# Optimization experiments

Hardware: AMD Instinct MI355X
Metric: run time of the kernel (lower is better)

Reference implementation:

```python
import jax, jax.numpy as jnp
import numpy as np

GRID_SIZE = 10
DEGREE = 3


def bspline_basis(x, grid_size=GRID_SIZE, degree=DEGREE):
    """Cox-de Boor B-spline basis on a uniform grid over [-1, 1].
    x: (...,) -> (..., grid_size + degree)
    """
    h = 2.0 / grid_size
    # extended knot vector, length grid_size + 2*degree + 1
    knots = jnp.arange(-degree, grid_size + degree + 1, dtype=x.dtype) * h - 1.0
    # keep inputs inside the grid support (standard KAN practice)
    x = jnp.clip(x, -1.0, 1.0 - 1e-6)
    xe = x[..., None]
    b = ((xe >= knots[:-1]) & (xe < knots[1:])).astype(x.dtype)  # degree-0, (..., K-1)
    for d in range(1, degree + 1):
        left = (xe - knots[: -(d + 1)]) / (knots[d:-1] - knots[: -(d + 1)]) * b[..., :-1]
        right = (knots[d + 1:] - xe) / (knots[d + 1:] - knots[1:-d]) * b[..., 1:]
        b = left + right
    return b  # (..., grid_size + degree)


def setup_inputs() -> dict:
    key = jax.random.key(0)
    k1, k2, k3 = jax.random.split(key, 3)
    B, S, IN, OUT, E = 4, 2048, 256, 256, 8
    n_basis = GRID_SIZE + DEGREE
    x = jax.random.normal(k1, (B, S, IN), dtype=jnp.float32)
    coeff = jax.random.normal(k2, (E, n_basis), dtype=jnp.float32) * 0.1
    gating_weights = jax.random.normal(k3, (IN, OUT, E), dtype=jnp.float32)
    return {"x": x, "coeff": coeff, "gating_weights": gating_weights}


def reference(x, coeff, gating_weights):
    # spline experts: elementwise basis eval, then per-expert linear combo
    basis = bspline_basis(x)                              # (B, S, I, n_basis)
    expert_outputs = jnp.einsum('bsin,en->bsie', basis, coeff)  # (B, S, I, E)
    gates = jax.nn.softmax(gating_weights, axis=-1)       # (I, O, E)
    out = jnp.einsum('bsie,ioe->bso', expert_outputs, gates)
    return out
```

## Files before the change

kernel.cpp:

```cpp
#include <hip/hip_runtime.h>

typedef __attribute__((ext_vector_type(8))) short short8;
typedef __attribute__((ext_vector_type(4))) float f32x4;

#define IN_DIM 256
#define OUT_DIM 256
#define NB 16
#define KDIM (IN_DIM * NB)
#define TM 128
#define TN 128
#define BK 64
#define KSPLIT 4
#define IPER (IN_DIM / KSPLIT)
#define STEPS (IPER / 4)

__device__ __forceinline__ unsigned short f2bf(float f) {
  union { float f; unsigned int u; } v; v.f = f;
  unsigned int r = v.u + 0x7fffu + ((v.u >> 16) & 1u);
  return (unsigned short)(r >> 16);
}

__device__ __forceinline__ void glds16(const void* g, void* l) {
  __builtin_amdgcn_global_load_lds((__attribute__((address_space(1))) const void*)g,
                                   (__attribute__((address_space(3))) void*)l, 16, 0, 0);
}

__device__ __forceinline__ void spline_row(float xv, unsigned* d) {
  float xc = fminf(fmaxf(xv, -1.0f), 1.0f - 1e-6f);
  float u = (xc + 1.0f) * 5.0f;
  int c = (int)u;
  c = c > 9 ? 9 : (c < 0 ? 0 : c);
  float tt = u - (float)c;
  float omt = 1.0f - tt;
  float t2 = tt * tt, t3 = t2 * tt;
  float b0 = omt * omt * omt * (1.0f / 6.0f);
  float b1 = (3.0f * t3 - 6.0f * t2 + 4.0f) * (1.0f / 6.0f);
  float b2 = (-3.0f * t3 + 3.0f * t2 + 3.0f * tt + 1.0f) * (1.0f / 6.0f);
  float b3 = t3 * (1.0f / 6.0f);
  unsigned h0 = f2bf(b0), h1 = f2bf(b1), h2 = f2bf(b2), h3 = f2bf(b3);
  const int a = c >> 1;
  const bool odd = (c & 1) != 0;
  unsigned p01 = h0 | (h1 << 16);
  unsigned p23 = h2 | (h3 << 16);
  unsigned A0 = odd ? (h0 << 16) : p01;
  unsigned A1 = odd ? (h1 | (h2 << 16)) : p23;
  unsigned A2 = odd ? h3 : 0u;
#pragma unroll
  for (int j = 0; j < 8; ++j) {
    unsigned v = (j == a) ? A0 : 0u;
    v = (j == a + 1) ? A1 : v;
    v = (j == a + 2) ? A2 : v;
    d[j] = v;
  }
}

__global__ __launch_bounds__(256) void kan_prep(const float* __restrict__ coeff,
                                                const float* __restrict__ gw,
                                                unsigned short* __restrict__ BmT,
                                                float* __restrict__ out) {
  __shared__ float csh[104];
  __shared__ unsigned short tile[16][256];
  const int t = threadIdx.x;
  {
    const int bid = blockIdx.y * 16 + blockIdx.x;
    float4 z; z.x = z.y = z.z = z.w = 0.f;
    float4* ob = (float4*)out;
#pragma unroll
    for (int j = 0; j < 8; ++j) ob[(size_t)bid * 2048 + j * 256 + t] = z;
  }
  if (t < 104) csh[t] = coeff[t];
  __syncthreads();
  const int otile = blockIdx.x, itile = blockIdx.y;
  const int il = t >> 4, ol = t & 15;
  const int i = itile * 16 + il;
  const int o = otile * 16 + ol;
  const float* g = gw + (size_t)(i * OUT_DIM + o) * 8;
  float4 g0 = *(const float4*)g;
  float4 g1 = *(const float4*)(g + 4);
  float ge[8] = {g0.x, g0.y, g0.z, g0.w, g1.x, g1.y, g1.z, g1.w};
  float mx = ge[0];
#pragma unroll
  for (int e = 1; e < 8; ++e) mx = fmaxf(mx, ge[e]);
  float p[8]; float s = 0.f;
#pragma unroll
  for (int e = 0; e < 8; ++e) { p[e] = __expf(ge[e] - mx); s += p[e]; }
  const float inv = 1.0f / s;
  unsigned short row[16];
#pragma unroll
  for (int n = 0; n < 13; ++n) {
    float w = 0.f;
#pragma unroll
    for (int e = 0; e < 8; ++e) w += p[e] * csh[e * 13 + n];
    row[n] = f2bf(w * inv);
  }
  row[13] = 0; row[14] = 0; row[15] = 0;
  int4* dst = (int4*)&tile[ol][il * 16];
  dst[0] = *(const int4*)&row[0];
  dst[1] = *(const int4*)&row[8];
  __syncthreads();
  const int oo = t >> 4, ck = t & 15;
  int4 v0 = *(const int4*)&tile[oo][ck * 16];
  int4 v1 = *(const int4*)&tile[oo][ck * 16 + 8];
  int4* out4 = (int4*)(BmT + (size_t)(otile * 16 + oo) * KDIM + itile * 256 + ck * 16);
  out4[0] = v0;
  out4[1] = v1;
}

#define STAGE_A(snext, buf) do {                                                   \
    const int p_ = (snext) & 1, h_ = ((snext) >> 1) & 1;                           \
    const char* xb_ = (const char*)&Xsh[0][0] + h_ * 4096;                         \
    float2 xv_ = *(const float2*)(xb_ + r * 32 + ((p_ ^ (r & 1)) << 4) + ph * 8);  \
    char* ab_ = (char*)&Ash[0][0] + (buf) * 16384 + r * 128;                       \
    const int m_ = r & 7;                                                          \
    unsigned d_[8];                                                                \
    spline_row(xv_.x, d_);                                                         \
    *(int4*)(ab_ + (((4 * ph + 0) ^ m_) << 4)) = *(const int4*)&d_[0];             \
    *(int4*)(ab_ + (((4 * ph + 1) ^ m_) << 4)) = *(const int4*)&d_[4];             \
    spline_row(xv_.y, d_);                                                         \
    *(int4*)(ab_ + (((4 * ph + 2) ^ m_) << 4)) = *(const int4*)&d_[0];             \
    *(int4*)(ab_ + (((4 * ph + 3) ^ m_) << 4)) = *(const int4*)&d_[4];             \
  } while (0)

__global__ __launch_bounds__(256, 2) void kan_gemm(const float* __restrict__ x,
                                                   const unsigned short* __restrict__ BmT,
                                                   float* __restrict__ out) {
  __shared__ unsigned short Ash[2][TM * BK];
  __shared__ unsigned short Bsh[2][TN * BK];
  __shared__ float Xsh[2][TM * 8];

  const int t = threadIdx.x;
  const int lane = t & 63;
  const int wave = t >> 6;
  const int wm = wave & 1, wn = wave >> 1;
  const int mb = blockIdx.x * TM;
  const int ob = blockIdx.y * TN;
  const int i0 = blockIdx.z * IPER;

  const int r = t & 127;
  const int ph = t >> 7;

  const int jsw = (t & 7) ^ ((t >> 3) & 7);
  const unsigned short* bgbase = BmT + (size_t)(ob + (t >> 3)) * KDIM + i0 * NB + jsw * 8;
  const int csw = (t & 1) ^ ((t >> 1) & 1);
  const float* xgbase = x + (size_t)(mb + (t >> 1)) * IN_DIM + i0 + csw * 4;

  char* const bl = (char*)&Bsh[0][0] + wave * 1024;
  char* const xl = (char*)&Xsh[0][0] + wave * 1024;

  f32x4 acc[4][4];
#pragma unroll
  for (int a = 0; a < 4; ++a)
#pragma unroll
    for (int b = 0; b < 4; ++b) acc[a][b] = (f32x4){0.f, 0.f, 0.f, 0.f};

  int aoff[4], boff[4];
#pragma unroll
  for (int f = 0; f < 4; ++f) {
    const int ro = wm * 64 + f * 16 + (lane & 15);
    aoff[f] = ro * 128 + ((((lane >> 4)) ^ (ro & 7)) << 4);
    const int bo = wn * 64 + f * 16 + (lane & 15);
    boff[f] = bo * 128 + ((((lane >> 4)) ^ (bo & 7)) << 4);
  }

  glds16(xgbase, xl);
#pragma unroll
  for (int q = 0; q < 4; ++q)
    glds16(bgbase + (size_t)q * 32 * KDIM, bl + q * 4096);
  asm volatile("s_waitcnt vmcnt(0)" ::: "memory");
  __syncthreads();
  STAGE_A(0, 0);

  for (int s = 0; s < STEPS; ++s) {
    __syncthreads();
    const int cur = s & 1;
    if (s + 1 < STEPS) {
#pragma unroll
      for (int q = 0; q < 4; ++q)
        glds16(bgbase + (size_t)(s + 1) * BK + (size_t)q * 32 * KDIM,
               bl + (1 - cur) * 16384 + q * 4096);
    }
    if (((s & 1) == 0) && (s + 2 < STEPS)) {
      const int g = (s >> 1) + 1;
      glds16(xgbase + g * 8, xl + (g & 1) * 4096);
    }
    const char* Ac = (const char*)&Ash[0][0] + cur * 16384;
    const char* Bc = (const char*)&Bsh[0][0] + cur * 16384;
    __builtin_amdgcn_s_setprio(1);
#pragma unroll
    for (int kc = 0; kc < 2; ++kc) {
      short8 af[4], bfr[4];
#pragma unroll
      for (int f = 0; f < 4; ++f) af[f] = *(const short8*)(Ac + (aoff[f] ^ (kc << 6)));
#pragma unroll
      for (int f = 0; f < 4; ++f) bfr[f] = *(const short8*)(Bc + (boff[f] ^ (kc << 6)));
#pragma unroll
      for (int mf = 0; mf < 4; ++mf)
#pragma unroll
        for (int nf = 0; nf < 4; ++nf)
          acc[mf][nf] = __builtin_amdgcn_mfma_f32_16x16x32_bf16(af[mf], bfr[nf], acc[mf][nf], 0, 0, 0);
    }
    __builtin_amdgcn_s_setprio(0);
    if (s + 1 < STEPS) STAGE_A(s + 1, 1 - cur);
  }

#pragma unroll
  for (int mf = 0; mf < 4; ++mf)
#pragma unroll
    for (int nf = 0; nf < 4; ++nf)
#pragma unroll
      for (int q = 0; q < 4; ++q) {
        int row = mb + wm * 64 + mf * 16 + ((lane >> 4) << 2) + q;
        int col = ob + wn * 64 + nf * 16 + (lane & 15);
        atomicAdd(out + (size_t)row * OUT_DIM + col, acc[mf][nf][q]);
      }
}

extern "C" void kernel_launch(void* const* d_in, const int* in_sizes, int n_in,
                              void* d_out, int out_size, void* d_ws, size_t ws_size,
                              hipStream_t stream) {
  const float* x     = (const float*)d_in[0];
  const float* coeff = (const float*)d_in[1];
  const float* gw    = (const float*)d_in[2];
  float* out = (float*)d_out;
  unsigned short* BmT = (unsigned short*)d_ws;

  kan_prep<<<dim3(16, 16), dim3(256), 0, stream>>>(coeff, gw, BmT, out);
  dim3 grid(8192 / TM, OUT_DIM / TN, KSPLIT);
  kan_gemm<<<grid, dim3(256), 0, stream>>>(x, BmT, out);
}
```

Before: 114.1 us.

## Drop split-K atomics; use small M tiles with full-K blocks and plain stores

Removes the K-split and atomic accumulation. Each block now handles a 32x128 output tile over the full input dimension and writes results with plain stores, so the output no longer needs zeroing in the prep kernel. The B operand is staged with a wider BK of 128. x is read directly from global memory per step instead of through LDS staging. The tiles are much smaller, which lowers MFMA reuse per block and increases redundant B-matrix loads across the larger number of blocks.

```diff
diff --git a/kernel.cpp b/kernel.cpp
--- a/kernel.cpp
+++ b/kernel.cpp
@@ -7,12 +7,12 @@
 #define OUT_DIM 256
 #define NB 16
 #define KDIM (IN_DIM * NB)
-#define TM 128
+#define TM 32
 #define TN 128
-#define BK 64
-#define KSPLIT 4
-#define IPER (IN_DIM / KSPLIT)
-#define STEPS (IPER / 4)
+#define BK 128
+#define STEPS (IN_DIM / 8)
+#define ABUF (TM * BK * 2)
+#define BBUF (TN * BK * 2)
 
 __device__ __forceinline__ unsigned short f2bf(float f) {
   union { float f; unsigned int u; } v; v.f = f;
@@ -56,18 +56,10 @@
 
 __global__ __launch_bounds__(256) void kan_prep(const float* __restrict__ coeff,
                                                 const float* __restrict__ gw,
-                                                unsigned short* __restrict__ BmT,
-                                                float* __restrict__ out) {
+                                                unsigned short* __restrict__ BmT) {
   __shared__ float csh[104];
   __shared__ unsigned short tile[16][256];
   const int t = threadIdx.x;
-  {
-    const int bid = blockIdx.y * 16 + blockIdx.x;
-    float4 z; z.x = z.y = z.z = z.w = 0.f;
-    float4* ob = (float4*)out;
-#pragma unroll
-    for (int j = 0; j < 8; ++j) ob[(size_t)bid * 2048 + j * 256 + t] = z;
-  }
   if (t < 104) csh[t] = coeff[t];
   __syncthreads();
   const int otile = blockIdx.x, itile = blockIdx.y;
@@ -106,112 +98,104 @@
   out4[1] = v1;
 }
 
-#define STAGE_A(snext, buf) do {                                                   \
-    const int p_ = (snext) & 1, h_ = ((snext) >> 1) & 1;                           \
-    const char* xb_ = (const char*)&Xsh[0][0] + h_ * 4096;                         \
-    float2 xv_ = *(const float2*)(xb_ + r * 32 + ((p_ ^ (r & 1)) << 4) + ph * 8);  \
-    char* ab_ = (char*)&Ash[0][0] + (buf) * 16384 + r * 128;                       \
-    const int m_ = r & 7;                                                          \
-    unsigned d_[8];                                                                \
-    spline_row(xv_.x, d_);                                                         \
-    *(int4*)(ab_ + (((4 * ph + 0) ^ m_) << 4)) = *(const int4*)&d_[0];             \
-    *(int4*)(ab_ + (((4 * ph + 1) ^ m_) << 4)) = *(const int4*)&d_[4];             \
-    spline_row(xv_.y, d_);                                                         \
-    *(int4*)(ab_ + (((4 * ph + 2) ^ m_) << 4)) = *(const int4*)&d_[0];             \
-    *(int4*)(ab_ + (((4 * ph + 3) ^ m_) << 4)) = *(const int4*)&d_[4];             \
-  } while (0)
-
 __global__ __launch_bounds__(256, 2) void kan_gemm(const float* __restrict__ x,
                                                    const unsigned short* __restrict__ BmT,
                                                    float* __restrict__ out) {
   __shared__ unsigned short Ash[2][TM * BK];
   __shared__ unsigned short Bsh[2][TN * BK];
-  __shared__ float Xsh[2][TM * 8];
 
   const int t = threadIdx.x;
   const int lane = t & 63;
   const int wave = t >> 6;
-  const int wm = wave & 1, wn = wave >> 1;
+  const int wn = wave;
   const int mb = blockIdx.x * TM;
   const int ob = blockIdx.y * TN;
-  const int i0 = blockIdx.z * IPER;
-
-  const int r = t & 127;
-  const int ph = t >> 7;
-
-  const int jsw = (t & 7) ^ ((t >> 3) & 7);
-  const unsigned short* bgbase = BmT + (size_t)(ob + (t >> 3)) * KDIM + i0 * NB + jsw * 8;
-  const int csw = (t & 1) ^ ((t >> 1) & 1);
-  const float* xgbase = x + (size_t)(mb + (t >> 1)) * IN_DIM + i0 + csw * 4;
-
+
+  const int r = t & 31;
+  const int il = t >> 5;
+  const float* xptr = x + (size_t)(mb + r) * IN_DIM + il;
+  char* const abase = (char*)&Ash[0][0] + r * 256;
+  const int msw = r & 7;
+  const int aw0 = ((2 * il + 0) ^ msw) << 4;
+  const int aw1 = ((2 * il + 1) ^ msw) << 4;
+
+  const unsigned short* bgbase =
+      BmT + (size_t)(ob + (t >> 4)) * KDIM + ((t & 15) ^ ((t >> 4) & 7)) * 8;
   char* const bl = (char*)&Bsh[0][0] + wave * 1024;
-  char* const xl = (char*)&Xsh[0][0] + wave * 1024;
-
-  f32x4 acc[4][4];
-#pragma unroll
-  for (int a = 0; a < 4; ++a)
-#pragma unroll
-    for (int b = 0; b < 4; ++b) acc[a][b] = (f32x4){0.f, 0.f, 0.f, 0.f};
-
-  int aoff[4], boff[4];
-#pragma unroll
-  for (int f = 0; f < 4; ++f) {
-    const int ro = wm * 64 + f * 16 + (lane & 15);
-    aoff[f] = ro * 128 + ((((lane >> 4)) ^ (ro & 7)) << 4);
-    const int bo = wn * 64 + f * 16 + (lane & 15);
-    boff[f] = bo * 128 + ((((lane >> 4)) ^ (bo & 7)) << 4);
-  }
-
-  glds16(xgbase, xl);
-#pragma unroll
-  for (int q = 0; q < 4; ++q)
-    glds16(bgbase + (size_t)q * 32 * KDIM, bl + q * 4096);
-  asm volatile("s_waitcnt vmcnt(0)" ::: "memory");
-  __syncthreads();
-  STAGE_A(0, 0);
+
+  f32x4 acc[2][2];
+#pragma unroll
+  for (int a = 0; a < 2; ++a)
+#pragma unroll
+    for (int b = 0; b < 2; ++b) acc[a][b] = (f32x4){0.f, 0.f, 0.f, 0.f};
+
+  int aoff[2], boff[2];
+#pragma unroll
+  for (int f = 0; f < 2; ++f) {
+    const int ro = f * 16 + (lane & 15);
+    aoff[f] = ro * 256 + (((lane >> 4) ^ (ro & 7)) << 4);
+    const int bo = wn * 32 + f * 16 + (lane & 15);
+    boff[f] = bo * 256 + (((lane >> 4) ^ (bo & 7)) << 4);
+  }
+
+  {
+#pragma unroll
+    for (int q = 0; q < 8; ++q)
+      glds16(bgbase + (size_t)q * 16 * KDIM, bl + q * 4096);
+    float xv = *xptr;
+    unsigned d[8];
+    spline_row(xv, d);
+    *(int4*)(abase + aw0) = *(const int4*)&d[0];
+    *(int4*)(abase + aw1) = *(const int4*)&d[4];
+    asm volatile("s_waitcnt vmcnt(0)" ::: "memory");
+  }
 
   for (int s = 0; s < STEPS; ++s) {
     __syncthreads();
     const int cur = s & 1;
+    float xn = 0.f;
     if (s + 1 < STEPS) {
-#pragma unroll
-      for (int q = 0; q < 4; ++q)
-        glds16(bgbase + (size_t)(s + 1) * BK + (size_t)q * 32 * KDIM,
-               bl + (1 - cur) * 16384 + q * 4096);
+      xn = xptr[(s + 1) * 8];
+#pragma unroll
+      for (int q = 0; q < 8; ++q)
+        glds16(bgbase + (size_t)(s + 1) * BK + (size_t)q * 16 * KDIM,
+               bl + (1 - cur) * BBUF + q * 4096);
     }
-    if (((s & 1) == 0) && (s + 2 < STEPS)) {
-      const int g = (s >> 1) + 1;
-      glds16(xgbase + g * 8, xl + (g & 1) * 4096);
-    }
-    const char* Ac = (const char*)&Ash[0][0] + cur * 16384;
-    const char* Bc = (const char*)&Bsh[0][0] + cur * 16384;
+    const char* Ac = (const char*)&Ash[0][0] + cur * ABUF;
+    const char* Bc = (const char*)&Bsh[0][0] + cur * BBUF;
     __builtin_amdgcn_s_setprio(1);
 #pragma unroll
-    for (int kc = 0; kc < 2; ++kc) {
-      short8 af[4], bfr[4];
-#pragma unroll
-      for (int f = 0; f < 4; ++f) af[f] = *(const short8*)(Ac + (aoff[f] ^ (kc << 6)));
-#pragma unroll
-      for (int f = 0; f < 4; ++f) bfr[f] = *(const short8*)(Bc + (boff[f] ^ (kc << 6)));
-#pragma unroll
-      for (int mf = 0; mf < 4; ++mf)
-#pragma unroll
-        for (int nf = 0; nf < 4; ++nf)
+    for (int kc = 0; kc < 4; ++kc) {
+      short8 af[2], bfr[2];
+#pragma unroll
+      for (int f = 0; f < 2; ++f) af[f] = *(const short8*)(Ac + (aoff[f] ^ (kc << 6)));
+#pragma unroll
+      for (int f = 0; f < 2; ++f) bfr[f] = *(const short8*)(Bc + (boff[f] ^ (kc << 6)));
+#pragma unroll
+      for (int mf = 0; mf < 2; ++mf)
+#pragma unroll
+        for (int nf = 0; nf < 2; ++nf)
           acc[mf][nf] = __builtin_amdgcn_mfma_f32_16x16x32_bf16(af[mf], bfr[nf], acc[mf][nf], 0, 0, 0);
     }
     __builtin_amdgcn_s_setprio(0);
-    if (s + 1 < STEPS) STAGE_A(s + 1, 1 - cur);
-  }
-
-#pragma unroll
-  for (int mf = 0; mf < 4; ++mf)
-#pragma unroll
-    for (int nf = 0; nf < 4; ++nf)
+    if (s + 1 < STEPS) {
+      unsigned d[8];
+      spline_row(xn, d);
+      char* an = abase + (1 - cur) * ABUF;
+      *(int4*)(an + aw0) = *(const int4*)&d[0];
+      *(int4*)(an + aw1) = *(const int4*)&d[4];
+    }
+  }
+
+#pragma unroll
+  for (int mf = 0; mf < 2; ++mf)
+#pragma unroll
+    for (int nf = 0; nf < 2; ++nf)
 #pragma unroll
       for (int q = 0; q < 4; ++q) {
-        int row = mb + wm * 64 + mf * 16 + ((lane >> 4) << 2) + q;
-        int col = ob + wn * 64 + nf * 16 + (lane & 15);
-        atomicAdd(out + (size_t)row * OUT_DIM + col, acc[mf][nf][q]);
+        int row = mb + mf * 16 + ((lane >> 4) << 2) + q;
+        int col = ob + wn * 32 + nf * 16 + (lane & 15);
+        out[(size_t)row * OUT_DIM + col] = acc[mf][nf][q];
       }
 }
 
@@ -224,7 +208,7 @@
   float* out = (float*)d_out;
   unsigned short* BmT = (unsigned short*)d_ws;
 
-  kan_prep<<<dim3(16, 16), dim3(256), 0, stream>>>(coeff, gw, BmT, out);
-  dim3 grid(8192 / TM, OUT_DIM / TN, KSPLIT);
+  kan_prep<<<dim3(16, 16), dim3(256), 0, stream>>>(coeff, gw, BmT);
+  dim3 grid(8192 / TM, OUT_DIM / TN);
   kan_gemm<<<grid, dim3(256), 0, stream>>>(x, BmT, out);
 }
```

New measurement: 105.1 us. -7.9%, faster.
